# Performance work log

Measured on AMD Instinct MI355X. Metric: run time of the kernel, lower is better.

## Reference

```python
import jax, jax.numpy as jnp
import numpy as np

N, Q, C, T = 32, 300, 92, 32  # batch, queries, classes, targets-per-image
L_CLS, L_IOU, L_L1 = 1.0, 2.0, 5.0


def _cxcywh_to_xyxy(b):
    cx, cy, w, h = b[..., 0], b[..., 1], b[..., 2], b[..., 3]
    return jnp.stack([cx - 0.5 * w, cy - 0.5 * h, cx + 0.5 * w, cy + 0.5 * h], axis=-1)


def _generalized_box_iou(a, b):
    # a: [P,4] xyxy, b: [M,4] xyxy -> [P,M]
    area_a = (a[:, 2] - a[:, 0]) * (a[:, 3] - a[:, 1])
    area_b = (b[:, 2] - b[:, 0]) * (b[:, 3] - b[:, 1])
    lt = jnp.maximum(a[:, None, :2], b[None, :, :2])
    rb = jnp.minimum(a[:, None, 2:], b[None, :, 2:])
    wh = jnp.clip(rb - lt, 0.0)
    inter = wh[..., 0] * wh[..., 1]
    union = area_a[:, None] + area_b[None, :] - inter
    iou = inter / union
    lt_c = jnp.minimum(a[:, None, :2], b[None, :, :2])
    rb_c = jnp.maximum(a[:, None, 2:], b[None, :, 2:])
    wh_c = jnp.clip(rb_c - lt_c, 0.0)
    area_c = wh_c[..., 0] * wh_c[..., 1]
    return iou - (area_c - union) / area_c


def _cost_matrix(pred_logits, pred_boxes, tgt_labels, tgt_boxes):
    out_prob = jax.nn.softmax(pred_logits.reshape(-1, C), axis=-1)  # [N*Q, C]
    out_bbox = pred_boxes.reshape(-1, 4)                            # [N*Q, 4]
    cost_class = -out_prob[:, tgt_labels]                           # [N*Q, N*T]
    cost_bbox = jnp.sum(jnp.abs(out_bbox[:, None, :] - tgt_boxes[None, :, :]), axis=-1)
    cost_giou = -_generalized_box_iou(_cxcywh_to_xyxy(out_bbox), _cxcywh_to_xyxy(tgt_boxes))
    cost = L_L1 * cost_bbox + L_CLS * cost_class + L_IOU * cost_giou
    return cost.reshape(N, Q, N * T)


def _lsa(cost):
    # Jonker-Volgenant shortest augmenting path (e-maxx), cost: [n, m], n <= m.
    # Returns col4row: for each row, the assigned column.
    n, m = cost.shape
    INF = np.inf
    u = np.zeros(n + 1)
    v = np.zeros(m + 1)
    p = np.zeros(m + 1, dtype=np.int64)   # p[j] = row assigned to column j (1-based)
    way = np.zeros(m + 1, dtype=np.int64)
    for i in range(1, n + 1):
        p[0] = i
        j0 = 0
        minv = np.full(m + 1, INF)
        used = np.zeros(m + 1, dtype=bool)
        while True:
            used[j0] = True
            i0 = p[j0]
            free = ~used[1:]
            cur = cost[i0 - 1] - u[i0] - v[1:]
            upd = free & (cur < minv[1:])
            minv[1:][upd] = cur[upd]
            way[1:][upd] = j0
            j1 = 1 + int(np.argmin(np.where(free, minv[1:], INF)))
            delta = minv[j1]
            used_idx = np.nonzero(used)[0]
            u[p[used_idx]] += delta
            v[used_idx] -= delta
            minv[1:][free] -= delta
            j0 = j1
            if p[j0] == 0:
                break
        while j0:
            j1 = way[j0]
            p[j0] = p[j1]
            j0 = j1
    ans = np.full(n, -1, dtype=np.int64)
    js = np.nonzero(p[1:])[0]
    ans[p[1:][js] - 1] = js
    return ans


def _multiplier(cost):
    c_np = np.asarray(jax.device_get(cost))  # [N, Q, N*T]
    mult = np.zeros_like(c_np)
    for i in range(N):
        block = c_np[i, :, i * T:(i + 1) * T]  # [Q, T], sample i's own targets
        q_of_t = _lsa(block.T)                 # for each target, matched query
        # NOTE: faithfully replicates the original code's `count = 0` reset,
        # so columns are indexed locally (first T columns of the global axis).
        mult[i, q_of_t, np.arange(T)] = 1.0
    return jnp.asarray(mult)


def setup_inputs() -> dict:
    key = jax.random.key(0)
    k1, k2, k3, k4 = jax.random.split(key, 4)
    return {
        "pred_logits": jax.random.normal(k1, (N, Q, C), dtype=jnp.float32),
        "pred_boxes": jax.random.uniform(k2, (N, Q, 4), dtype=jnp.float32),
        "tgt_labels": jax.random.randint(k3, (N * T,), 0, C, dtype=jnp.int64),
        "tgt_boxes": jax.random.uniform(k4, (N * T, 4), dtype=jnp.float32),
    }


def reference(pred_logits, pred_boxes, tgt_labels, tgt_boxes):
    cost = _cost_matrix(pred_logits, pred_boxes, tgt_labels, tgt_boxes)
    mult = _multiplier(cost)
    return jnp.sum(cost * mult)
```

## Files before the change

kernel.cpp:

```cpp
#include <hip/hip_runtime.h>
#include <cfloat>
#include <cmath>

#define Nn 32
#define Qq 300
#define Cc 92
#define Tt 32
#define KCOLS 5
#define LSTRIDE 93
#define GSZ 10
#define GCOLS 30
#define AUCTION_ROUNDS 10
#define AUCTION_EPS 1e-3f
#define NTHREADS 1024

__device__ inline float wave_min_bcast(float x) {
#define DPPMIN(ctrl) { int _t = __builtin_amdgcn_update_dpp( \
        __float_as_int(x), __float_as_int(x), ctrl, 0xf, 0xf, false); \
        x = fminf(x, __int_as_float(_t)); }
    DPPMIN(0x111) DPPMIN(0x112) DPPMIN(0x114) DPPMIN(0x118)
    DPPMIN(0x142) DPPMIN(0x143)
#undef DPPMIN
    return __int_as_float(__builtin_amdgcn_readlane(__float_as_int(x), 63));
}

__device__ inline int sel5i(const int a[KCOLS], int k) {
    int r = a[0];
    if (k == 1) r = a[1];
    if (k == 2) r = a[2];
    if (k == 3) r = a[3];
    if (k == 4) r = a[4];
    return r;
}

__device__ inline float readlane_f(float v, int lane) {
    return __int_as_float(__builtin_amdgcn_readlane(__float_as_int(v), lane));
}

__device__ inline void softmax_lds(const float* __restrict__ srow,
                                   float& mx, float& inv_s) {
    float m0 = -FLT_MAX, m1 = -FLT_MAX, m2 = -FLT_MAX, m3 = -FLT_MAX;
#pragma unroll
    for (int c = 0; c < Cc; c += 4) {
        m0 = fmaxf(m0, srow[c + 0]);
        m1 = fmaxf(m1, srow[c + 1]);
        m2 = fmaxf(m2, srow[c + 2]);
        m3 = fmaxf(m3, srow[c + 3]);
    }
    const float m = fmaxf(fmaxf(m0, m1), fmaxf(m2, m3));
    float s0 = 0.f, s1 = 0.f, s2 = 0.f, s3 = 0.f;
#pragma unroll
    for (int c = 0; c < Cc; c += 4) {
        s0 += __expf(srow[c + 0] - m);
        s1 += __expf(srow[c + 1] - m);
        s2 += __expf(srow[c + 2] - m);
        s3 += __expf(srow[c + 3] - m);
    }
    mx = m; inv_s = 1.f / ((s0 + s1) + (s2 + s3));
}

__device__ inline float det_cost(float cx, float cy, float w, float h,
                                 float bcx, float bcy, float bw, float bh,
                                 float cls) {
    const float ax0 = cx - 0.5f * w, ay0 = cy - 0.5f * h;
    const float ax1 = cx + 0.5f * w, ay1 = cy + 0.5f * h;
    const float areaA = (ax1 - ax0) * (ay1 - ay0);

    const float l1 = fabsf(cx - bcx) + fabsf(cy - bcy) +
                     fabsf(w - bw) + fabsf(h - bh);

    const float bx0 = bcx - 0.5f * bw, by0 = bcy - 0.5f * bh;
    const float bx1 = bcx + 0.5f * bw, by1 = bcy + 0.5f * bh;
    const float areaB = (bx1 - bx0) * (by1 - by0);

    const float ltx = fmaxf(ax0, bx0), lty = fmaxf(ay0, by0);
    const float rbx = fminf(ax1, bx1), rby = fminf(ay1, by1);
    const float iw = fmaxf(rbx - ltx, 0.f), ih = fmaxf(rby - lty, 0.f);
    const float inter = iw * ih;
    const float uni = areaA + areaB - inter;
    const float iou = inter / uni;

    const float ex0 = fminf(ax0, bx0), ey0 = fminf(ay0, by0);
    const float ex1 = fmaxf(ax1, bx1), ey1 = fmaxf(ay1, by1);
    const float areaC = fmaxf(ex1 - ex0, 0.f) * fmaxf(ey1 - ey0, 0.f);
    const float giou = iou - (areaC - uni) / areaC;

    return 5.f * l1 + cls - 2.f * giou;
}

__global__ __launch_bounds__(NTHREADS) void fused_kernel(
    const float* __restrict__ logits,
    const float* __restrict__ pboxes,
    const int*   __restrict__ tlabels,
    const float* __restrict__ tboxes,
    float* __restrict__ out)
{
    const int b = blockIdx.x;
    const int tid = threadIdx.x;

    extern __shared__ float s_lg[];
    __shared__ float s_diag[Tt * Qq];
    __shared__ float s_tb[Tt * 4];
    __shared__ int   s_tl[Tt];
    __shared__ int   pairs[Tt];
    __shared__ float2 s_mxis[Qq];
    __shared__ float s_v[Qq];
    __shared__ float s_u[Tt + 1];
    __shared__ int   s_colrow[Qq];
    __shared__ unsigned long long s_bid64[Qq];
    __shared__ float s_pm1[320], s_pm2[320];
    __shared__ int   s_pa[320];
    __shared__ unsigned s_mask;

    if (tid < Tt * 4) s_tb[tid] = tboxes[b * Tt * 4 + tid];
    if (tid < Tt)     s_tl[tid] = tlabels[b * Tt + tid];
    if (tid < Qq)     { s_v[tid] = 0.f; s_colrow[tid] = 0; }
    if (tid == 0)     s_mask = 0xffffffffu;

    {
        const float4* lgb = reinterpret_cast<const float4*>(
            logits + (size_t)b * Qq * Cc);
#pragma unroll 4
        for (int g = tid; g < Qq * 23; g += NTHREADS) {
            const float4 v = lgb[g];
            const int r = g / 23, c4 = (g - r * 23) * 4;
            float* dst = &s_lg[r * LSTRIDE + c4];
            dst[0] = v.x; dst[1] = v.y; dst[2] = v.z; dst[3] = v.w;
        }
    }
    __syncthreads();

    if (tid < Qq) {
        float mx, inv_s;
        softmax_lds(&s_lg[tid * LSTRIDE], mx, inv_s);
        s_mxis[tid] = make_float2(mx, inv_s);
    }
    __syncthreads();

    for (int e = tid; e < Tt * Qq; e += NTHREADS) {
        const int t = e / Qq, q = e - t * Qq;
        const float2 mi = s_mxis[q];
        const float* srow = &s_lg[q * LSTRIDE];
        const float cls = -__expf(srow[s_tl[t]] - mi.x) * mi.y;
        const float4 pbv = reinterpret_cast<const float4*>(pboxes)[b * Qq + q];
        s_diag[e] = det_cost(pbv.x, pbv.y, pbv.z, pbv.w,
                             s_tb[t * 4 + 0], s_tb[t * 4 + 1],
                             s_tb[t * 4 + 2], s_tb[t * 4 + 3], cls);
    }
    __syncthreads();

    {
        const int grp = tid / GSZ;
        const int g   = tid - grp * GSZ;
        for (int round = 0; round < AUCTION_ROUNDS; ++round) {
            const unsigned msk = s_mask;
            if (msk == 0) break;
            for (int j = tid; j < Qq; j += NTHREADS) s_bid64[j] = 0ull;

            if (tid < 320 && (msk & (1u << grp))) {
                const float* rowp = &s_diag[grp * Qq];
                float m1 = INFINITY, m2 = INFINITY; int a1 = 0;
                const int c0 = g * GCOLS;
#pragma unroll
                for (int j = 0; j < GCOLS; ++j) {
                    const int cidx = c0 + j;
                    const float c = rowp[cidx] - s_v[cidx];
                    if (c < m1) { m2 = m1; m1 = c; a1 = cidx + 1; }
                    else if (c < m2) m2 = c;
                }
                s_pm1[tid] = m1; s_pm2[tid] = m2; s_pa[tid] = a1;
            }
            __syncthreads();

            float g1 = 0.f, g2 = 0.f; int j1 = 0;
            unsigned long long mypk = 0ull;
            if (tid < Tt && (msk & (1u << tid))) {
                float best = INFINITY, second = INFINITY, bm2 = INFINITY;
                int ba = 0;
                const int base = tid * GSZ;
#pragma unroll
                for (int q = 0; q < GSZ; ++q) {
                    const float v = s_pm1[base + q];
                    if (v < best) {
                        second = best; best = v;
                        ba = s_pa[base + q]; bm2 = s_pm2[base + q];
                    } else if (v < second) second = v;
                }
                g1 = best; g2 = fminf(second, bm2); j1 = ba;
                mypk = ((unsigned long long)(__float_as_uint(g2 - g1) + 1u) << 32)
                       | (unsigned)(0xffffffffu - (unsigned)(tid + 1));
                atomicMax(&s_bid64[j1 - 1], mypk);
            }
            __syncthreads();

            if (tid < Tt && (msk & (1u << tid))) {
                const int row = tid + 1;
                const float eps = (round < 2) ? 0.f : AUCTION_EPS;
                if (s_bid64[j1 - 1] == mypk) {
                    const int old = s_colrow[j1 - 1];
                    s_colrow[j1 - 1] = row;
                    s_v[j1 - 1] -= (g2 - g1) + eps;
                    s_u[row] = g2;
                    atomicAnd(&s_mask, ~(1u << tid));
                    if (old) atomicOr(&s_mask, 1u << (old - 1));
                } else {
                    s_u[row] = g1;
                }
            }
            __syncthreads();
        }
    }

    if (tid >= 64) return;
    const int lane = tid;
    const bool inval4 = (lane + 256) >= Qq;

    float u_reg = (lane >= 1 && lane <= Tt) ? s_u[lane] : 0.f;
    float v_r[KCOLS]; int p_r[KCOLS];
#pragma unroll
    for (int k = 0; k < KCOLS; ++k) {
        const int j = lane + 64 * k;
        v_r[k] = (j < Qq) ? s_v[j] : 0.f;
        p_r[k] = (j < Qq) ? s_colrow[j] : 0;
    }

    for (unsigned rem = s_mask; rem; rem &= rem - 1) {
        const int i = __ffs(rem);

        float minv_r[KCOLS], vmask[KCOLS], am[KCOLS];
        int way_r[KCOLS];
#pragma unroll
        for (int k = 0; k < KCOLS; ++k) {
            minv_r[k] = FLT_MAX; way_r[k] = 0;
            const bool inv = (k == 4) && inval4;
            vmask[k] = inv ? -INFINITY : v_r[k];
            am[k]    = inv ?  INFINITY : 0.f;
        }
        float markg = 0.f;
        int   ent = 0;
        int   j0 = 0, i0 = i;
        float du = 0.f - readlane_f(u_reg, i);
        int   jfinal = 0;
        float Dfinal = 0.f;

        const float* rowp = &s_diag[(i0 - 1) * Qq + lane];
        float c0 = rowp[0], c1 = rowp[64], c2 = rowp[128], c3 = rowp[192],
              c4 = rowp[256];

        while (true) {
            const float cc[KCOLS] = {c0, c1, c2, c3, c4};
            float sv[KCOLS];
#pragma unroll
            for (int k = 0; k < KCOLS; ++k) {
                const float cur = (cc[k] + du) - vmask[k];
                const bool lt = cur < minv_r[k];
                way_r[k]  = lt ? j0  : way_r[k];
                minv_r[k] = lt ? cur : minv_r[k];
                sv[k] = minv_r[k] + am[k];
            }
            float val = sv[0];
            int   kb  = 0;
#pragma unroll
            for (int k = 1; k < KCOLS; ++k)
                if (sv[k] < val) { val = sv[k]; kb = k; }

            const float gmin = wave_min_bcast(val);
            const unsigned long long mask = __ballot(val == gmin);
            const int src = __ffsll((long long)mask) - 1;
            const int colid = lane + 1 + (kb << 6);
            const int pk = (sel5i(p_r, kb) << 16) | colid;
            const int got = __builtin_amdgcn_readlane(pk, src);
            const int j1   = got & 0xffff;
            const int rowm = got >> 16;

            const int k1 = (j1 - 1) >> 6;
            const bool own = (lane == ((j1 - 1) & 63));
#pragma unroll
            for (int k = 0; k < KCOLS; ++k)
                if (own && k == k1) { vmask[k] = -INFINITY; am[k] = INFINITY; }

            if (rowm == 0) { jfinal = j1; Dfinal = gmin; break; }

            i0 = rowm; j0 = j1;
            rowp = &s_diag[(i0 - 1) * Qq + lane];
            c0 = rowp[0]; c1 = rowp[64]; c2 = rowp[128]; c3 = rowp[192];
            c4 = rowp[256];
            du = gmin - readlane_f(u_reg, i0);
            markg = (lane == rowm) ? gmin : markg;
            ent   = (lane == rowm) ? 1    : ent;
        }

#pragma unroll
        for (int k = 0; k < KCOLS; ++k) {
            bool usedk = (am[k] == INFINITY);
            if (k == 4) usedk = usedk && !inval4;
            v_r[k] -= usedk ? (Dfinal - minv_r[k]) : 0.f;
        }
        u_reg += (lane == i) ? Dfinal : (ent ? (Dfinal - markg) : 0.f);

        int jj = jfinal;
        while (jj) {
            const int ow = (jj - 1) & 63, kk = (jj - 1) >> 6;
            const int jprev = __builtin_amdgcn_readlane(sel5i(way_r, kk), ow);
            int pnew;
            if (jprev == 0) pnew = i;
            else pnew = __builtin_amdgcn_readlane(sel5i(p_r, (jprev - 1) >> 6),
                                                  (jprev - 1) & 63);
            const bool own = (lane == ow);
#pragma unroll
            for (int k = 0; k < KCOLS; ++k) if (own && k == kk) p_r[k] = pnew;
            jj = jprev;
        }
    }

#pragma unroll
    for (int k = 0; k < KCOLS; ++k)
        if (p_r[k]) pairs[p_r[k] - 1] = lane + 64 * k;
    __threadfence_block();

    float part = 0.f;
    if (lane < Tt) {
        const int q = pairs[lane];
        const float2 mi = s_mxis[q];
        const float* srow = &s_lg[q * LSTRIDE];
        const float cls = -__expf(srow[tlabels[lane]] - mi.x) * mi.y;
        const float4 pbv = reinterpret_cast<const float4*>(pboxes)[b * Qq + q];
        const float4 tbv = reinterpret_cast<const float4*>(tboxes)[lane];
        part = det_cost(pbv.x, pbv.y, pbv.z, pbv.w,
                        tbv.x, tbv.y, tbv.z, tbv.w, cls);
    }
    for (int off = 32; off > 0; off >>= 1) part += __shfl_down(part, off);
    if (lane == 0) atomicAdd(out, part);
}

extern "C" void kernel_launch(void* const* d_in, const int* in_sizes, int n_in,
                              void* d_out, int out_size, void* d_ws, size_t ws_size,
                              hipStream_t stream) {
    const float* logits  = (const float*)d_in[0];
    const float* pboxes  = (const float*)d_in[1];
    const int*   tlabels = (const int*)d_in[2];
    const float* tboxes  = (const float*)d_in[3];
    float* out = (float*)d_out;

    (void)hipMemsetAsync(out, 0, sizeof(float), stream);
    const size_t lg_bytes = (size_t)Qq * LSTRIDE * sizeof(float);
    fused_kernel<<<Nn, NTHREADS, lg_bytes, stream>>>(logits, pboxes, tlabels,
                                                     tboxes, out);
}
```

Baseline: 80.70 us.

## Split fused matcher into cost, auction, and finish kernels with workspace handoff

Replaces the single 32-block fused kernel with three launches. A cost kernel spreads softmax and the per-sample cost diagonal over 256 blocks (8 query slices per sample). An auction kernel then runs the bidding rounds, and a finish kernel completes the shortest-augmenting-path step and the sum. The aim is to use more CUs for the cost stage, which previously ran on only 32 blocks, and to shrink per-block LDS and thread counts. In exchange it adds two extra launches and round-trips the cost matrix and auction state through global workspace memory.

```diff
diff --git a/kernel.cpp b/kernel.cpp
--- a/kernel.cpp
+++ b/kernel.cpp
@@ -7,12 +7,21 @@
 #define Cc 92
 #define Tt 32
 #define KCOLS 5
-#define LSTRIDE 93
 #define GSZ 10
 #define GCOLS 30
 #define AUCTION_ROUNDS 10
 #define AUCTION_EPS 1e-3f
-#define NTHREADS 1024
+
+#define SLICES 8
+#define RPS 38
+#define CTHREADS 256
+#define ATHREADS 320
+#define FTHREADS 256
+
+#define DIAG_OFF   0
+#define MXIS_OFF   (Nn * Tt * Qq)
+#define STATE_OFF  (MXIS_OFF + 2 * Nn * Qq)
+#define STATE_STRIDE 640
 
 __device__ inline float wave_min_bcast(float x) {
 #define DPPMIN(ctrl) { int _t = __builtin_amdgcn_update_dpp( \
@@ -37,31 +46,9 @@
     return __int_as_float(__builtin_amdgcn_readlane(__float_as_int(v), lane));
 }
 
-__device__ inline void softmax_lds(const float* __restrict__ srow,
-                                   float& mx, float& inv_s) {
-    float m0 = -FLT_MAX, m1 = -FLT_MAX, m2 = -FLT_MAX, m3 = -FLT_MAX;
-#pragma unroll
-    for (int c = 0; c < Cc; c += 4) {
-        m0 = fmaxf(m0, srow[c + 0]);
-        m1 = fmaxf(m1, srow[c + 1]);
-        m2 = fmaxf(m2, srow[c + 2]);
-        m3 = fmaxf(m3, srow[c + 3]);
-    }
-    const float m = fmaxf(fmaxf(m0, m1), fmaxf(m2, m3));
-    float s0 = 0.f, s1 = 0.f, s2 = 0.f, s3 = 0.f;
-#pragma unroll
-    for (int c = 0; c < Cc; c += 4) {
-        s0 += __expf(srow[c + 0] - m);
-        s1 += __expf(srow[c + 1] - m);
-        s2 += __expf(srow[c + 2] - m);
-        s3 += __expf(srow[c + 3] - m);
-    }
-    mx = m; inv_s = 1.f / ((s0 + s1) + (s2 + s3));
-}
-
-__device__ inline float det_cost(float cx, float cy, float w, float h,
-                                 float bcx, float bcy, float bw, float bh,
-                                 float cls) {
+__device__ inline float det_cost_real(float cx, float cy, float w, float h,
+                                      float bcx, float bcy, float bw, float bh,
+                                      float cls) {
     const float ax0 = cx - 0.5f * w, ay0 = cy - 0.5f * h;
     const float ax1 = cx + 0.5f * w, ay1 = cy + 0.5f * h;
     const float areaA = (ax1 - ax0) * (ay1 - ay0);
@@ -88,143 +75,201 @@
     return 5.f * l1 + cls - 2.f * giou;
 }
 
-__global__ __launch_bounds__(NTHREADS) void fused_kernel(
+__global__ __launch_bounds__(CTHREADS) void cost_kernel(
     const float* __restrict__ logits,
     const float* __restrict__ pboxes,
     const int*   __restrict__ tlabels,
     const float* __restrict__ tboxes,
+    float* __restrict__ ws)
+{
+    const int bs = blockIdx.x;
+    const int b = bs >> 3, s = bs & 7;
+    const int q0 = s * RPS;
+    const int nq = min(RPS, Qq - q0);
+
+    __shared__ float2 s_mxis[RPS];
+    __shared__ float  s_tb[Tt * 4];
+    __shared__ int    s_tl[Tt];
+
+    const int tid = threadIdx.x;
+    if (tid < Tt * 4) s_tb[tid] = tboxes[b * Tt * 4 + tid];
+    if (tid < Tt)     s_tl[tid] = tlabels[b * Tt + tid];
+
+    const int r = tid >> 2, j = tid & 3;
+    if (r < nq) {
+        const float* row = logits + ((size_t)(b * Qq) + q0 + r) * Cc;
+        float mj = -FLT_MAX;
+#pragma unroll
+        for (int c = 0; c < Cc; c += 4) mj = fmaxf(mj, row[c + j]);
+        const float ma = fmaxf(mj, __shfl_xor(mj, 1, 4));
+        const float mx = fmaxf(ma, __shfl_xor(ma, 2, 4));
+        float sj = 0.f;
+#pragma unroll
+        for (int c = 0; c < Cc; c += 4) sj += __expf(row[c + j] - mx);
+        const float sa   = sj + __shfl_xor(sj, 1, 4);
+        const float ssum = sa + __shfl_xor(sa, 2, 4);
+        if (j == 0) {
+            const float2 mi = make_float2(mx, 1.f / ssum);
+            s_mxis[r] = mi;
+            reinterpret_cast<float2*>(ws + MXIS_OFF)[b * Qq + q0 + r] = mi;
+        }
+    }
+    __syncthreads();
+
+    float* diagb = ws + DIAG_OFF + (size_t)b * (Tt * Qq);
+    for (int e = tid; e < Tt * RPS; e += CTHREADS) {
+        const int t = e / RPS, lq = e - t * RPS;
+        const int q = q0 + lq;
+        if (q < Qq) {
+            const float2 mi = s_mxis[lq];
+            const float cls =
+                -__expf(logits[((size_t)(b * Qq) + q) * Cc + s_tl[t]] - mi.x) * mi.y;
+            const float4 pbv = reinterpret_cast<const float4*>(pboxes)[b * Qq + q];
+            diagb[t * Qq + q] = det_cost_real(pbv.x, pbv.y, pbv.z, pbv.w,
+                                              s_tb[t * 4 + 0], s_tb[t * 4 + 1],
+                                              s_tb[t * 4 + 2], s_tb[t * 4 + 3], cls);
+        }
+    }
+}
+
+__global__ __launch_bounds__(ATHREADS) void auction_kernel(
+    float* __restrict__ ws)
+{
+    const int b = blockIdx.x;
+    const int tid = threadIdx.x;
+
+    __shared__ float s_diag[Tt * Qq];
+    __shared__ float s_v[Qq];
+    __shared__ float s_u[Tt + 1];
+    __shared__ int   s_colrow[Qq];
+    __shared__ unsigned long long s_bid64[Qq];
+    __shared__ float s_pm1[ATHREADS], s_pm2[ATHREADS];
+    __shared__ int   s_pa[ATHREADS];
+    __shared__ unsigned s_mask;
+
+    {
+        const float4* src = reinterpret_cast<const float4*>(
+            ws + DIAG_OFF + (size_t)b * (Tt * Qq));
+        float4* dst = reinterpret_cast<float4*>(s_diag);
+#pragma unroll 2
+        for (int g = tid; g < (Tt * Qq) / 4; g += ATHREADS) dst[g] = src[g];
+    }
+    if (tid < Qq)  { s_v[tid] = 0.f; s_colrow[tid] = 0; }
+    if (tid == 0)  s_mask = 0xffffffffu;
+    __syncthreads();
+
+    const int grp = tid / GSZ;
+    const int g   = tid - grp * GSZ;
+    for (int round = 0; round < AUCTION_ROUNDS; ++round) {
+        const unsigned msk = s_mask;
+        if (msk == 0) break;
+        for (int jj = tid; jj < Qq; jj += ATHREADS) s_bid64[jj] = 0ull;
+
+        if (grp < Tt && (msk & (1u << grp))) {
+            const float* rowp = &s_diag[grp * Qq];
+            float m1 = INFINITY, m2 = INFINITY; int a1 = 0;
+            const int c0 = g * GCOLS;
+#pragma unroll
+            for (int jj = 0; jj < GCOLS; ++jj) {
+                const int cidx = c0 + jj;
+                const float c = rowp[cidx] - s_v[cidx];
+                if (c < m1) { m2 = m1; m1 = c; a1 = cidx + 1; }
+                else if (c < m2) m2 = c;
+            }
+            s_pm1[tid] = m1; s_pm2[tid] = m2; s_pa[tid] = a1;
+        }
+        __syncthreads();
+
+        float g1 = 0.f, g2 = 0.f; int j1 = 0;
+        unsigned long long mypk = 0ull;
+        if (tid < Tt && (msk & (1u << tid))) {
+            float best = INFINITY, second = INFINITY, bm2 = INFINITY;
+            int ba = 0;
+            const int base = tid * GSZ;
+#pragma unroll
+            for (int q = 0; q < GSZ; ++q) {
+                const float v = s_pm1[base + q];
+                if (v < best) {
+                    second = best; best = v;
+                    ba = s_pa[base + q]; bm2 = s_pm2[base + q];
+                } else if (v < second) second = v;
+            }
+            g1 = best; g2 = fminf(second, bm2); j1 = ba;
+            mypk = ((unsigned long long)(__float_as_uint(g2 - g1) + 1u) << 32)
+                   | (unsigned)(0xffffffffu - (unsigned)(tid + 1));
+            atomicMax(&s_bid64[j1 - 1], mypk);
+        }
+        __syncthreads();
+
+        if (tid < Tt && (msk & (1u << tid))) {
+            const int row = tid + 1;
+            const float eps = (round < 2) ? 0.f : AUCTION_EPS;
+            if (s_bid64[j1 - 1] == mypk) {
+                const int old = s_colrow[j1 - 1];
+                s_colrow[j1 - 1] = row;
+                s_v[j1 - 1] -= (g2 - g1) + eps;
+                s_u[row] = g2;
+                atomicAnd(&s_mask, ~(1u << tid));
+                if (old) atomicOr(&s_mask, 1u << (old - 1));
+            } else {
+                s_u[row] = g1;
+            }
+        }
+        __syncthreads();
+    }
+
+    __syncthreads();
+    float* st  = ws + STATE_OFF + (size_t)b * STATE_STRIDE;
+    int*   sti = reinterpret_cast<int*>(st + 334);
+    for (int jj = tid; jj < Qq; jj += ATHREADS) {
+        st[jj]  = s_v[jj];
+        sti[jj] = s_colrow[jj];
+    }
+    if (tid >= 1 && tid <= Tt) st[300 + tid] = s_u[tid];
+    if (tid == 0) *reinterpret_cast<unsigned*>(st + 634) = s_mask;
+}
+
+__global__ __launch_bounds__(FTHREADS) void finish_kernel(
+    const float* __restrict__ logits,
+    const float* __restrict__ pboxes,
+    const int*   __restrict__ tlabels,
+    const float* __restrict__ tboxes,
+    const float* __restrict__ ws,
     float* __restrict__ out)
 {
     const int b = blockIdx.x;
     const int tid = threadIdx.x;
 
-    extern __shared__ float s_lg[];
     __shared__ float s_diag[Tt * Qq];
-    __shared__ float s_tb[Tt * 4];
-    __shared__ int   s_tl[Tt];
     __shared__ int   pairs[Tt];
-    __shared__ float2 s_mxis[Qq];
-    __shared__ float s_v[Qq];
-    __shared__ float s_u[Tt + 1];
-    __shared__ int   s_colrow[Qq];
-    __shared__ unsigned long long s_bid64[Qq];
-    __shared__ float s_pm1[320], s_pm2[320];
-    __shared__ int   s_pa[320];
-    __shared__ unsigned s_mask;
-
-    if (tid < Tt * 4) s_tb[tid] = tboxes[b * Tt * 4 + tid];
-    if (tid < Tt)     s_tl[tid] = tlabels[b * Tt + tid];
-    if (tid < Qq)     { s_v[tid] = 0.f; s_colrow[tid] = 0; }
-    if (tid == 0)     s_mask = 0xffffffffu;
 
     {
-        const float4* lgb = reinterpret_cast<const float4*>(
-            logits + (size_t)b * Qq * Cc);
-#pragma unroll 4
-        for (int g = tid; g < Qq * 23; g += NTHREADS) {
-            const float4 v = lgb[g];
-            const int r = g / 23, c4 = (g - r * 23) * 4;
-            float* dst = &s_lg[r * LSTRIDE + c4];
-            dst[0] = v.x; dst[1] = v.y; dst[2] = v.z; dst[3] = v.w;
-        }
+        const float4* src = reinterpret_cast<const float4*>(
+            ws + DIAG_OFF + (size_t)b * (Tt * Qq));
+        float4* dst = reinterpret_cast<float4*>(s_diag);
+#pragma unroll 2
+        for (int g = tid; g < (Tt * Qq) / 4; g += FTHREADS) dst[g] = src[g];
     }
     __syncthreads();
-
-    if (tid < Qq) {
-        float mx, inv_s;
-        softmax_lds(&s_lg[tid * LSTRIDE], mx, inv_s);
-        s_mxis[tid] = make_float2(mx, inv_s);
-    }
-    __syncthreads();
-
-    for (int e = tid; e < Tt * Qq; e += NTHREADS) {
-        const int t = e / Qq, q = e - t * Qq;
-        const float2 mi = s_mxis[q];
-        const float* srow = &s_lg[q * LSTRIDE];
-        const float cls = -__expf(srow[s_tl[t]] - mi.x) * mi.y;
-        const float4 pbv = reinterpret_cast<const float4*>(pboxes)[b * Qq + q];
-        s_diag[e] = det_cost(pbv.x, pbv.y, pbv.z, pbv.w,
-                             s_tb[t * 4 + 0], s_tb[t * 4 + 1],
-                             s_tb[t * 4 + 2], s_tb[t * 4 + 3], cls);
-    }
-    __syncthreads();
-
-    {
-        const int grp = tid / GSZ;
-        const int g   = tid - grp * GSZ;
-        for (int round = 0; round < AUCTION_ROUNDS; ++round) {
-            const unsigned msk = s_mask;
-            if (msk == 0) break;
-            for (int j = tid; j < Qq; j += NTHREADS) s_bid64[j] = 0ull;
-
-            if (tid < 320 && (msk & (1u << grp))) {
-                const float* rowp = &s_diag[grp * Qq];
-                float m1 = INFINITY, m2 = INFINITY; int a1 = 0;
-                const int c0 = g * GCOLS;
-#pragma unroll
-                for (int j = 0; j < GCOLS; ++j) {
-                    const int cidx = c0 + j;
-                    const float c = rowp[cidx] - s_v[cidx];
-                    if (c < m1) { m2 = m1; m1 = c; a1 = cidx + 1; }
-                    else if (c < m2) m2 = c;
-                }
-                s_pm1[tid] = m1; s_pm2[tid] = m2; s_pa[tid] = a1;
-            }
-            __syncthreads();
-
-            float g1 = 0.f, g2 = 0.f; int j1 = 0;
-            unsigned long long mypk = 0ull;
-            if (tid < Tt && (msk & (1u << tid))) {
-                float best = INFINITY, second = INFINITY, bm2 = INFINITY;
-                int ba = 0;
-                const int base = tid * GSZ;
-#pragma unroll
-                for (int q = 0; q < GSZ; ++q) {
-                    const float v = s_pm1[base + q];
-                    if (v < best) {
-                        second = best; best = v;
-                        ba = s_pa[base + q]; bm2 = s_pm2[base + q];
-                    } else if (v < second) second = v;
-                }
-                g1 = best; g2 = fminf(second, bm2); j1 = ba;
-                mypk = ((unsigned long long)(__float_as_uint(g2 - g1) + 1u) << 32)
-                       | (unsigned)(0xffffffffu - (unsigned)(tid + 1));
-                atomicMax(&s_bid64[j1 - 1], mypk);
-            }
-            __syncthreads();
-
-            if (tid < Tt && (msk & (1u << tid))) {
-                const int row = tid + 1;
-                const float eps = (round < 2) ? 0.f : AUCTION_EPS;
-                if (s_bid64[j1 - 1] == mypk) {
-                    const int old = s_colrow[j1 - 1];
-                    s_colrow[j1 - 1] = row;
-                    s_v[j1 - 1] -= (g2 - g1) + eps;
-                    s_u[row] = g2;
-                    atomicAnd(&s_mask, ~(1u << tid));
-                    if (old) atomicOr(&s_mask, 1u << (old - 1));
-                } else {
-                    s_u[row] = g1;
-                }
-            }
-            __syncthreads();
-        }
-    }
 
     if (tid >= 64) return;
     const int lane = tid;
     const bool inval4 = (lane + 256) >= Qq;
 
-    float u_reg = (lane >= 1 && lane <= Tt) ? s_u[lane] : 0.f;
+    const float* st  = ws + STATE_OFF + (size_t)b * STATE_STRIDE;
+    const int*   sti = reinterpret_cast<const int*>(st + 334);
+
+    float u_reg = (lane >= 1 && lane <= Tt) ? st[300 + lane] : 0.f;
     float v_r[KCOLS]; int p_r[KCOLS];
 #pragma unroll
     for (int k = 0; k < KCOLS; ++k) {
-        const int j = lane + 64 * k;
-        v_r[k] = (j < Qq) ? s_v[j] : 0.f;
-        p_r[k] = (j < Qq) ? s_colrow[j] : 0;
-    }
-
-    for (unsigned rem = s_mask; rem; rem &= rem - 1) {
+        const int jj = lane + 64 * k;
+        v_r[k] = (jj < Qq) ? st[jj]  : 0.f;
+        p_r[k] = (jj < Qq) ? sti[jj] : 0;
+    }
+    const unsigned mask0 = *reinterpret_cast<const unsigned*>(st + 634);
+
+    for (unsigned rem = mask0; rem; rem &= rem - 1) {
         const int i = __ffs(rem);
 
         float minv_r[KCOLS], vmask[KCOLS], am[KCOLS];
@@ -321,13 +366,14 @@
     float part = 0.f;
     if (lane < Tt) {
         const int q = pairs[lane];
-        const float2 mi = s_mxis[q];
-        const float* srow = &s_lg[q * LSTRIDE];
-        const float cls = -__expf(srow[tlabels[lane]] - mi.x) * mi.y;
+        const float2 mi =
+            reinterpret_cast<const float2*>(ws + MXIS_OFF)[b * Qq + q];
+        const float cls =
+            -__expf(logits[((size_t)(b * Qq) + q) * Cc + tlabels[lane]] - mi.x) * mi.y;
         const float4 pbv = reinterpret_cast<const float4*>(pboxes)[b * Qq + q];
         const float4 tbv = reinterpret_cast<const float4*>(tboxes)[lane];
-        part = det_cost(pbv.x, pbv.y, pbv.z, pbv.w,
-                        tbv.x, tbv.y, tbv.z, tbv.w, cls);
+        part = det_cost_real(pbv.x, pbv.y, pbv.z, pbv.w,
+                             tbv.x, tbv.y, tbv.z, tbv.w, cls);
     }
     for (int off = 32; off > 0; off >>= 1) part += __shfl_down(part, off);
     if (lane == 0) atomicAdd(out, part);
@@ -341,9 +387,12 @@
     const int*   tlabels = (const int*)d_in[2];
     const float* tboxes  = (const float*)d_in[3];
     float* out = (float*)d_out;
+    float* ws  = (float*)d_ws;
 
     (void)hipMemsetAsync(out, 0, sizeof(float), stream);
-    const size_t lg_bytes = (size_t)Qq * LSTRIDE * sizeof(float);
-    fused_kernel<<<Nn, NTHREADS, lg_bytes, stream>>>(logits, pboxes, tlabels,
-                                                     tboxes, out);
-}
+    cost_kernel<<<Nn * SLICES, CTHREADS, 0, stream>>>(logits, pboxes, tlabels,
+                                                      tboxes, ws);
+    auction_kernel<<<Nn, ATHREADS, 0, stream>>>(ws);
+    finish_kernel<<<Nn, FTHREADS, 0, stream>>>(logits, pboxes, tlabels,
+                                               tboxes, ws, out);
+}
```

New measurement: 81.62 us. Within noise of the previous version (+1.1%).
